# Performance work log

Hardware: AMD Instinct MI355X
Metric: run time of the kernel (lower is better)

The kernel has to match this reference:

```python
import jax, jax.numpy as jnp
import numpy as np

N_NODES = 100000
N_EDGES = 3200000
D_NODE = 5            # per-node feature dim
D_IN = 2 * D_NODE     # 10, MLP input dim
D_HID = D_IN * 5      # 50, HIDDEN_DIM_MULTIPLIER = 5


def setup_inputs() -> dict:
    key = jax.random.key(0)
    ks = jax.random.split(key, 8)
    x = jax.random.normal(ks[0], (N_NODES, D_NODE), dtype=jnp.float32)
    edge_index = jax.random.randint(ks[1], (2, N_EDGES), 0, N_NODES, dtype=jnp.int64)
    s1 = 1.0 / np.sqrt(D_IN)
    s2 = 1.0 / np.sqrt(D_HID)
    W1 = jax.random.uniform(ks[2], (D_IN, D_HID), jnp.float32, -s1, s1)
    b1 = jax.random.uniform(ks[3], (D_HID,), jnp.float32, -s1, s1)
    W2 = jax.random.uniform(ks[4], (D_HID, D_HID), jnp.float32, -s2, s2)
    b2 = jax.random.uniform(ks[5], (D_HID,), jnp.float32, -s2, s2)
    W3 = jax.random.uniform(ks[6], (D_HID, 1), jnp.float32, -s2, s2)
    b3 = jax.random.uniform(ks[7], (1,), jnp.float32, -s2, s2)
    return {"x": x, "edge_index": edge_index, "W1": W1, "b1": b1,
            "W2": W2, "b2": b2, "W3": W3, "b3": b3}


def reference(x, edge_index, W1, b1, W2, b2, W3, b3):
    # gather src/tgt node features and concat -> [E, 2*D_NODE]
    ef = jnp.concatenate([x[edge_index[0]], x[edge_index[1]]], axis=-1)
    h = jax.nn.relu(ef @ W1 + b1)
    h = jax.nn.relu(h @ W2 + b2)
    return jax.nn.sigmoid(h @ W3 + b3)  # [E, 1]
```

## Files before the change

kernel.cpp:

```cpp
#include <hip/hip_runtime.h>
#include <hip/hip_bf16.h>

typedef short bf16x8 __attribute__((ext_vector_type(8)));
typedef float f32x4  __attribute__((ext_vector_type(4)));

__device__ inline ushort f2bf(float f) {
    union { float f; uint u; } v; v.f = f;
    uint r = (v.u + 0x7FFFu + ((v.u >> 16) & 1u)) >> 16;
    return (ushort)r;
}
__device__ inline uint packbf(float a, float b) {
    float2 t; t.x = a; t.y = b;
    __hip_bfloat162 h = __float22bfloat162_rn(t);
    union { __hip_bfloat162 h; uint u; } cv; cv.h = h; return cv.u;
}

#define LDS_FENCE() asm volatile("s_waitcnt lgkmcnt(0)" ::: "memory")

__global__ __launch_bounds__(256, 2) void edge_mlp_mfma2(
    const float* __restrict__ x,
    const int* __restrict__ ei,
    const float* __restrict__ W1, const float* __restrict__ b1,
    const float* __restrict__ W2, const float* __restrict__ b2,
    const float* __restrict__ W3, const float* __restrict__ b3,
    float* __restrict__ out, int E, int num_tiles)
{
    __shared__ ushort lds_ef[4][32][56];

    const int tid  = threadIdx.x;
    const int w    = tid >> 6;
    const int lane = tid & 63;
    const int c    = lane & 15;
    const int g    = lane >> 4;

    {
        uint* p = (uint*)&lds_ef[w][0][0];
        #pragma unroll
        for (int i = 0; i < 14; ++i) p[lane + 64 * i] = 0;
    }

    bf16x8 w1tf[4];
    #pragma unroll
    for (int mt = 0; mt < 4; ++mt) {
        #pragma unroll
        for (int d = 0; d < 8; ++d) {
            int k  = 8 * g + d;
            int r1 = (k < 5) ? k : (k >= 6 && k < 11) ? k - 1 : -1;
            int j  = 16 * mt + c;
            float v = (r1 >= 0 && j < 50) ? W1[r1 * 50 + j] : 0.f;
            w1tf[mt][d] = (short)f2bf(v);
        }
    }
    bf16x8 w2tf[2][4];
    #pragma unroll
    for (int t = 0; t < 2; ++t) {
        #pragma unroll
        for (int mt = 0; mt < 4; ++mt) {
            #pragma unroll
            for (int d = 0; d < 8; ++d) {
                int hid1 = 16 * (2 * t + (d >> 2)) + 4 * g + (d & 3);
                int j    = 16 * mt + c;
                float v = (hid1 < 50 && j < 50) ? W2[hid1 * 50 + j] : 0.f;
                w2tf[t][mt][d] = (short)f2bf(v);
            }
        }
    }
    float b1c[4][4], b2c[4][4], w3c[4][4];
    #pragma unroll
    for (int mt = 0; mt < 4; ++mt)
        #pragma unroll
        for (int r = 0; r < 4; ++r) {
            int h = 16 * mt + 4 * g + r;
            b1c[mt][r] = (h < 50) ? b1[h] : 0.f;
            b2c[mt][r] = (h < 50) ? b2[h] : 0.f;
            w3c[mt][r] = (h < 50) ? W3[h] : 0.f;
        }
    const float b3s = b3[0];

    for (int bt = blockIdx.x; bt < num_tiles; bt += gridDim.x) {
        const int e0 = bt * 128 + w * 32;

        {
            int el = lane & 31;
            int wh = lane >> 5;
            int ge = e0 + el;
            if (ge >= E) ge = 0;
            int idx = ei[(size_t)wh * (size_t)E + (size_t)ge];
            const float* xr = x + (size_t)idx * 5;
            float f0 = xr[0], f1 = xr[1], f2 = xr[2], f3 = xr[3], f4 = xr[4];
            uint* dst = (uint*)&lds_ef[w][el][wh * 6];
            dst[0] = packbf(f0, f1);
            dst[1] = packbf(f2, f3);
            dst[2] = packbf(f4, 0.f);
        }
        LDS_FENCE();

        #pragma unroll
        for (int ms = 0; ms < 2; ++ms) {
            bf16x8 aEF = *(const bf16x8*)&lds_ef[w][ms * 16 + c][8 * g];

            f32x4 hT[4];
            #pragma unroll
            for (int mt = 0; mt < 4; ++mt) {
                f32x4 z = {0.f, 0.f, 0.f, 0.f};
                hT[mt] = __builtin_amdgcn_mfma_f32_16x16x32_bf16(w1tf[mt], aEF, z, 0, 0, 0);
            }

            uint pk[4][2];
            #pragma unroll
            for (int mt = 0; mt < 4; ++mt) {
                float v0 = fmaxf(hT[mt][0] + b1c[mt][0], 0.f);
                float v1 = fmaxf(hT[mt][1] + b1c[mt][1], 0.f);
                float v2 = fmaxf(hT[mt][2] + b1c[mt][2], 0.f);
                float v3 = fmaxf(hT[mt][3] + b1c[mt][3], 0.f);
                pk[mt][0] = packbf(v0, v1);
                pk[mt][1] = packbf(v2, v3);
            }
            union { uint u[4]; bf16x8 v; } uu;
            uu.u[0] = pk[0][0]; uu.u[1] = pk[0][1];
            uu.u[2] = pk[1][0]; uu.u[3] = pk[1][1];
            bf16x8 bB0 = uu.v;
            uu.u[0] = pk[2][0]; uu.u[1] = pk[2][1];
            uu.u[2] = pk[3][0]; uu.u[3] = pk[3][1];
            bf16x8 bB1 = uu.v;

            f32x4 h2T[4];
            #pragma unroll
            for (int mt = 0; mt < 4; ++mt) {
                f32x4 z = {0.f, 0.f, 0.f, 0.f};
                h2T[mt] = __builtin_amdgcn_mfma_f32_16x16x32_bf16(w2tf[0][mt], bB0, z, 0, 0, 0);
                h2T[mt] = __builtin_amdgcn_mfma_f32_16x16x32_bf16(w2tf[1][mt], bB1, h2T[mt], 0, 0, 0);
            }

            float p = 0.f;
            #pragma unroll
            for (int mt = 0; mt < 4; ++mt) {
                #pragma unroll
                for (int r = 0; r < 4; ++r) {
                    float t = fmaxf(h2T[mt][r] + b2c[mt][r], 0.f);
                    p = fmaf(t, w3c[mt][r], p);
                }
            }
            p += __shfl_xor(p, 16);
            p += __shfl_xor(p, 32);

            if (g == 0) {
                int eo = e0 + ms * 16 + c;
                if (eo < E) {
                    float zz = p + b3s;
                    out[eo] = 1.f / (1.f + __expf(-zz));
                }
            }
        }
    }
}

extern "C" void kernel_launch(void* const* d_in, const int* in_sizes, int n_in,
                              void* d_out, int out_size, void* d_ws, size_t ws_size,
                              hipStream_t stream) {
    const float* x  = (const float*)d_in[0];
    const int*   ei = (const int*)d_in[1];
    const float* W1 = (const float*)d_in[2];
    const float* b1 = (const float*)d_in[3];
    const float* W2 = (const float*)d_in[4];
    const float* b2 = (const float*)d_in[5];
    const float* W3 = (const float*)d_in[6];
    const float* b3 = (const float*)d_in[7];
    float* out = (float*)d_out;

    int E = in_sizes[1] / 2;
    int num_tiles = (E + 127) / 128;
    int grid = num_tiles < 2048 ? num_tiles : 2048;
    edge_mlp_mfma2<<<grid, 256, 0, stream>>>(x, ei, W1, b1, W2, b2, W3, b3,
                                             out, E, num_tiles);
}
```

Measured before the change: 80.89 us.

## Prepack node features to bf16 rows and fold biases into MFMA weights

Adds a pre-pass kernel that converts node features to 16-byte bf16 rows with a constant-one slot, so each lane gathers its MFMA operand with a single vector load straight into registers instead of staging through LDS. Biases b1 and b2 are folded into the weight fragments through the constant-one channel, which removes the per-element bias adds. Occupancy hint is raised to 4 blocks per CU. The cost is an extra kernel launch and a workspace pass over the node array, plus some extra bf16 rounding of the biases.

Result: slower. 84.14 us (+4.0%).

```diff
diff --git a/kernel.cpp b/kernel.cpp
--- a/kernel.cpp
+++ b/kernel.cpp
@@ -15,43 +15,52 @@
     union { __hip_bfloat162 h; uint u; } cv; cv.h = h; return cv.u;
 }
 
-#define LDS_FENCE() asm volatile("s_waitcnt lgkmcnt(0)" ::: "memory")
+__global__ __launch_bounds__(256) void pack_x_kernel(
+    const float* __restrict__ x, uint4* __restrict__ xp, int N)
+{
+    int i = blockIdx.x * blockDim.x + threadIdx.x;
+    if (i > N) return;
+    uint4 o = {0u, 0u, 0u, 0u};
+    if (i < N) {
+        const float* r = x + (size_t)i * 5;
+        o.x = packbf(r[0], r[1]);
+        o.y = packbf(r[2], r[3]);
+        o.z = packbf(r[4], 1.0f);
+    }
+    xp[i] = o;
+}
 
-__global__ __launch_bounds__(256, 2) void edge_mlp_mfma2(
-    const float* __restrict__ x,
+__global__ __launch_bounds__(256, 4) void edge_mlp_mfma3(
+    const uint4* __restrict__ xp,
     const int* __restrict__ ei,
     const float* __restrict__ W1, const float* __restrict__ b1,
     const float* __restrict__ W2, const float* __restrict__ b2,
     const float* __restrict__ W3, const float* __restrict__ b3,
-    float* __restrict__ out, int E, int num_tiles)
+    float* __restrict__ out, int E, int N, int num_tiles)
 {
-    __shared__ ushort lds_ef[4][32][56];
-
     const int tid  = threadIdx.x;
     const int w    = tid >> 6;
     const int lane = tid & 63;
     const int c    = lane & 15;
     const int g    = lane >> 4;
 
-    {
-        uint* p = (uint*)&lds_ef[w][0][0];
-        #pragma unroll
-        for (int i = 0; i < 14; ++i) p[lane + 64 * i] = 0;
-    }
-
-    bf16x8 w1tf[4];
+    bf16x8 w1f[4];
     #pragma unroll
     for (int mt = 0; mt < 4; ++mt) {
         #pragma unroll
         for (int d = 0; d < 8; ++d) {
-            int k  = 8 * g + d;
-            int r1 = (k < 5) ? k : (k >= 6 && k < 11) ? k - 1 : -1;
-            int j  = 16 * mt + c;
-            float v = (r1 >= 0 && j < 50) ? W1[r1 * 50 + j] : 0.f;
-            w1tf[mt][d] = (short)f2bf(v);
+            int k = 8 * g + d;
+            int j = 16 * mt + c;
+            float v = 0.f;
+            if (j < 50) {
+                if (k < 5)                 v = W1[k * 50 + j];
+                else if (k == 5)           v = b1[j];
+                else if (k >= 8 && k < 13) v = W1[(k - 3) * 50 + j];
+            } else if (j == 50 && k == 5)  v = 1.0f;
+            w1f[mt][d] = (short)f2bf(v);
         }
     }
-    bf16x8 w2tf[2][4];
+    bf16x8 w2f[2][4];
     #pragma unroll
     for (int t = 0; t < 2; ++t) {
         #pragma unroll
@@ -60,19 +69,21 @@
             for (int d = 0; d < 8; ++d) {
                 int hid1 = 16 * (2 * t + (d >> 2)) + 4 * g + (d & 3);
                 int j    = 16 * mt + c;
-                float v = (hid1 < 50 && j < 50) ? W2[hid1 * 50 + j] : 0.f;
-                w2tf[t][mt][d] = (short)f2bf(v);
+                float v = 0.f;
+                if (j < 50) {
+                    if (hid1 < 50)       v = W2[hid1 * 50 + j];
+                    else if (hid1 == 50) v = b2[j];
+                }
+                w2f[t][mt][d] = (short)f2bf(v);
             }
         }
     }
-    float b1c[4][4], b2c[4][4], w3c[4][4];
+    float w3c[4][4];
     #pragma unroll
     for (int mt = 0; mt < 4; ++mt)
         #pragma unroll
         for (int r = 0; r < 4; ++r) {
             int h = 16 * mt + 4 * g + r;
-            b1c[mt][r] = (h < 50) ? b1[h] : 0.f;
-            b2c[mt][r] = (h < 50) ? b2[h] : 0.f;
             w3c[mt][r] = (h < 50) ? W3[h] : 0.f;
         }
     const float b3s = b3[0];
@@ -80,39 +91,35 @@
     for (int bt = blockIdx.x; bt < num_tiles; bt += gridDim.x) {
         const int e0 = bt * 128 + w * 32;
 
-        {
-            int el = lane & 31;
-            int wh = lane >> 5;
-            int ge = e0 + el;
-            if (ge >= E) ge = 0;
-            int idx = ei[(size_t)wh * (size_t)E + (size_t)ge];
-            const float* xr = x + (size_t)idx * 5;
-            float f0 = xr[0], f1 = xr[1], f2 = xr[2], f3 = xr[3], f4 = xr[4];
-            uint* dst = (uint*)&lds_ef[w][el][wh * 6];
-            dst[0] = packbf(f0, f1);
-            dst[1] = packbf(f2, f3);
-            dst[2] = packbf(f4, 0.f);
+        bf16x8 aEF[2];
+        #pragma unroll
+        for (int ms = 0; ms < 2; ++ms) {
+            int e   = e0 + ms * 16 + c;
+            int idx = N;
+            if (g < 2) {
+                int ee = (e < E) ? e : 0;
+                idx = ei[(size_t)g * (size_t)E + (size_t)ee];
+            }
+            union { uint4 q; bf16x8 v; } u;
+            u.q = xp[idx];
+            aEF[ms] = u.v;
         }
-        LDS_FENCE();
 
         #pragma unroll
         for (int ms = 0; ms < 2; ++ms) {
-            bf16x8 aEF = *(const bf16x8*)&lds_ef[w][ms * 16 + c][8 * g];
-
             f32x4 hT[4];
             #pragma unroll
             for (int mt = 0; mt < 4; ++mt) {
                 f32x4 z = {0.f, 0.f, 0.f, 0.f};
-                hT[mt] = __builtin_amdgcn_mfma_f32_16x16x32_bf16(w1tf[mt], aEF, z, 0, 0, 0);
+                hT[mt] = __builtin_amdgcn_mfma_f32_16x16x32_bf16(w1f[mt], aEF[ms], z, 0, 0, 0);
             }
-
             uint pk[4][2];
             #pragma unroll
             for (int mt = 0; mt < 4; ++mt) {
-                float v0 = fmaxf(hT[mt][0] + b1c[mt][0], 0.f);
-                float v1 = fmaxf(hT[mt][1] + b1c[mt][1], 0.f);
-                float v2 = fmaxf(hT[mt][2] + b1c[mt][2], 0.f);
-                float v3 = fmaxf(hT[mt][3] + b1c[mt][3], 0.f);
+                float v0 = fmaxf(hT[mt][0], 0.f);
+                float v1 = fmaxf(hT[mt][1], 0.f);
+                float v2 = fmaxf(hT[mt][2], 0.f);
+                float v3 = fmaxf(hT[mt][3], 0.f);
                 pk[mt][0] = packbf(v0, v1);
                 pk[mt][1] = packbf(v2, v3);
             }
@@ -128,8 +135,8 @@
             #pragma unroll
             for (int mt = 0; mt < 4; ++mt) {
                 f32x4 z = {0.f, 0.f, 0.f, 0.f};
-                h2T[mt] = __builtin_amdgcn_mfma_f32_16x16x32_bf16(w2tf[0][mt], bB0, z, 0, 0, 0);
-                h2T[mt] = __builtin_amdgcn_mfma_f32_16x16x32_bf16(w2tf[1][mt], bB1, h2T[mt], 0, 0, 0);
+                h2T[mt] = __builtin_amdgcn_mfma_f32_16x16x32_bf16(w2f[0][mt], bB0, z, 0, 0, 0);
+                h2T[mt] = __builtin_amdgcn_mfma_f32_16x16x32_bf16(w2f[1][mt], bB1, h2T[mt], 0, 0, 0);
             }
 
             float p = 0.f;
@@ -137,7 +144,7 @@
             for (int mt = 0; mt < 4; ++mt) {
                 #pragma unroll
                 for (int r = 0; r < 4; ++r) {
-                    float t = fmaxf(h2T[mt][r] + b2c[mt][r], 0.f);
+                    float t = fmaxf(h2T[mt][r], 0.f);
                     p = fmaf(t, w3c[mt][r], p);
                 }
             }
@@ -145,10 +152,10 @@
             p += __shfl_xor(p, 32);
 
             if (g == 0) {
-                int eo = e0 + ms * 16 + c;
-                if (eo < E) {
+                int e = e0 + ms * 16 + c;
+                if (e < E) {
                     float zz = p + b3s;
-                    out[eo] = 1.f / (1.f + __expf(-zz));
+                    out[e] = 1.f / (1.f + __expf(-zz));
                 }
             }
         }
@@ -169,8 +176,13 @@
     float* out = (float*)d_out;
 
     int E = in_sizes[1] / 2;
+    int N = in_sizes[0] / 5;
+
+    uint4* xp = (uint4*)d_ws;
+    pack_x_kernel<<<(N + 1 + 255) / 256, 256, 0, stream>>>(x, xp, N);
+
     int num_tiles = (E + 127) / 128;
     int grid = num_tiles < 2048 ? num_tiles : 2048;
-    edge_mlp_mfma2<<<grid, 256, 0, stream>>>(x, ei, W1, b1, W2, b2, W3, b3,
-                                             out, E, num_tiles);
+    edge_mlp_mfma3<<<grid, 256, 0, stream>>>(xp, ei, W1, b1, W2, b2, W3, b3,
+                                             out, E, N, num_tiles);
 }
```
